# Kernel optimization log

Measured on AMD Instinct MI355X. Metric: run time of the kernel, lower is better.

## Reference

```python
import jax, jax.numpy as jnp
import numpy as np

B, L, E = 4, 2048, 1024
H, DQ, DV = 8, 128, 128
SCALE = 1.0 / np.sqrt(DQ).astype(np.float32)


def setup_inputs() -> dict:
    key = jax.random.key(0)
    ks = jax.random.split(key, 6)
    return {
        "qInputs": jax.random.normal(ks[0], (B, L, E), dtype=jnp.float32),
        "kvInputs": jax.random.normal(ks[1], (B, L, E), dtype=jnp.float32),
        "mask": jnp.zeros((B, H, L, L), dtype=jnp.bool_),
        "W_Q": jax.random.normal(ks[2], (E, H * DQ), dtype=jnp.float32) * 0.02,
        "W_K": jax.random.normal(ks[3], (E, H * DQ), dtype=jnp.float32) * 0.02,
        "W_V": jax.random.normal(ks[4], (E, H * DV), dtype=jnp.float32) * 0.02,
        "W_fc": jax.random.normal(ks[5], (H * DV, E), dtype=jnp.float32) * 0.02,
    }


def reference(qInputs, kvInputs, mask, W_Q, W_K, W_V, W_fc):
    b, lq, _ = qInputs.shape
    lk = kvInputs.shape[1]
    # Projections -> [B, H, L, D]
    Q = (qInputs @ W_Q).reshape(b, lq, H, DQ).transpose(0, 2, 1, 3)
    K = (kvInputs @ W_K).reshape(b, lk, H, DQ).transpose(0, 2, 1, 3)
    V = (kvInputs @ W_V).reshape(b, lk, H, DV).transpose(0, 2, 1, 3)
    # Scaled dot-product with additive mask fill of -1e9
    scores = jnp.einsum("bhqd,bhkd->bhqk", Q, K) * SCALE
    scores = jnp.where(mask, jnp.float32(-1e9), scores)
    attn = jax.nn.softmax(scores, axis=-1)
    ctx = jnp.einsum("bhqk,bhkd->bhqd", attn, V)
    ctx = ctx.transpose(0, 2, 1, 3).reshape(b, lq, H * DV)
    return ctx @ W_fc
```

## Files before the change

### kernel.cpp

```cpp
#include <hip/hip_runtime.h>
#include <stdint.h>

#define LQ 2048
#define EDIM 1024
#define HN 8
#define DH 128
#define BATCH 4
#define SCALE_LOG2E 0.12753785051263942f

typedef short bf16x8 __attribute__((ext_vector_type(8)));
typedef float f32x4 __attribute__((ext_vector_type(4)));
typedef unsigned short u16;
typedef unsigned short u16x4 __attribute__((ext_vector_type(4)));

__device__ __forceinline__ u16 f2bf(float f) {
  union { float f; uint32_t u; } c; c.f = f;
  uint32_t u = c.u;
  return (u16)((u + 0x7fffu + ((u >> 16) & 1u)) >> 16);
}

__device__ __forceinline__ void async16(const void* g, void* l) {
  __builtin_amdgcn_global_load_lds((const __attribute__((address_space(1))) void*)g,
                                   (__attribute__((address_space(3))) void*)l, 16, 0, 0);
}

__device__ __forceinline__ uint32_t lds_b(const u16* p) {
  return (uint32_t)(uintptr_t)(__attribute__((address_space(3))) const u16*)p;
}
__device__ __forceinline__ void ldsr4_issue(bf16x8& d0, bf16x8& d1, bf16x8& d2, bf16x8& d3,
                                            uint32_t a0, uint32_t a1, uint32_t a2, uint32_t a3) {
  asm volatile("ds_read_b128 %0, %4\n\t"
               "ds_read_b128 %1, %5\n\t"
               "ds_read_b128 %2, %6\n\t"
               "ds_read_b128 %3, %7"
               : "=&v"(d0), "=&v"(d1), "=&v"(d2), "=&v"(d3)
               : "v"(a0), "v"(a1), "v"(a2), "v"(a3));
}
template <int N>
__device__ __forceinline__ void lgkm_wait_sb() {
  asm volatile("s_waitcnt lgkmcnt(%0)" :: "n"(N) : "memory");
  __builtin_amdgcn_sched_barrier(0);
}
__device__ __forceinline__ uint32_t cvtpk(float lo, float hi) {
  uint32_t r;
  asm("v_cvt_pk_bf16_f32 %0, %1, %2" : "=v"(r) : "v"(lo), "v"(hi));
  return r;
}
__device__ __forceinline__ void plane_swap(uint32_t& a, uint32_t& b) {
#if __has_builtin(__builtin_amdgcn_permlane32_swap) && __has_builtin(__builtin_amdgcn_permlane16_swap)
  auto r1 = __builtin_amdgcn_permlane32_swap(a, b, false, false);
  auto r2 = __builtin_amdgcn_permlane16_swap(r1[0], r1[1], false, false);
  a = r2[0];
  b = r2[1];
#else
  asm("s_nop 1\n\t"
      "v_permlane32_swap_b32 %0, %1\n\t"
      "s_nop 1\n\t"
      "v_permlane16_swap_b32 %0, %1\n\t"
      "s_nop 1"
      : "+v"(a), "+v"(b));
#endif
}

__global__ __launch_bounds__(256) void prep_kernel(const float* __restrict__ qIn, const float* __restrict__ kvIn,
                                                   const float* __restrict__ w0, const float* __restrict__ w1,
                                                   const float* __restrict__ w2, const float* __restrict__ w3,
                                                   u16* __restrict__ oq, u16* __restrict__ okv,
                                                   u16* __restrict__ o0, u16* __restrict__ o1,
                                                   u16* __restrict__ o2, u16* __restrict__ o3) {
  __shared__ float tile[32][33];
  const int bid = blockIdx.x;
  const int t = threadIdx.x;
  if (bid < 16384) {
    const float* in = (bid >= 8192) ? kvIn : qIn;
    u16* out = (bid >= 8192) ? okv : oq;
    size_t i = (size_t)(bid & 8191) * 256 + t;
    float4 v = ((const float4*)in)[i];
    u16x4 o;
    o.x = f2bf(v.x); o.y = f2bf(v.y); o.z = f2bf(v.z); o.w = f2bf(v.w);
    ((u16x4*)out)[i] = o;
  } else {
    const int idx = bid - 16384;
    const int z = idx >> 10;
    const int rem = idx & 1023;
    const float* in; u16* out;
    switch (z) {
      case 0: in = w0; out = o0; break;
      case 1: in = w1; out = o1; break;
      case 2: in = w2; out = o2; break;
      default: in = w3; out = o3; break;
    }
    const int tx = t & 31, ty = t >> 5;
    const int x0 = (rem & 31) * 32;
    const int y0 = (rem >> 5) * 32;
#pragma unroll
    for (int j = 0; j < 32; j += 8)
      tile[ty + j][tx] = in[(size_t)(y0 + ty + j) * EDIM + x0 + tx];
    __syncthreads();
#pragma unroll
    for (int j = 0; j < 32; j += 8)
      out[(size_t)(x0 + ty + j) * EDIM + (y0 + tx)] = f2bf(tile[tx][ty + j]);
  }
}

struct GemmCore {
  template <typename EpiF>
  static __device__ __forceinline__ void run(const u16* __restrict__ A, const u16* __restrict__ Bt,
                                             int m0, int n0, u16* As, u16* Bs, EpiF epi) {
    const int tid = threadIdx.x;
    const int l = tid & 63;
    const int w = tid >> 6;
    const int wm = (w >> 1) * 64;
    const int wn = (w & 1) * 64;
    const int fm = l & 15;
    const int q4 = l >> 4;
    const int f7 = fm & 7;
    f32x4 acc[4][4] = {};
    for (int k0 = 0; k0 < EDIM; k0 += 64) {
      __syncthreads();
#pragma unroll
      for (int ii = 0; ii < 4; ++ii) {
        const int rloc = w * 32 + ii * 8 + (l >> 3);
        const int cs = (l & 7) ^ (rloc & 7);
        async16(A + (size_t)(m0 + rloc) * EDIM + k0 + cs * 8, &As[(w * 32 + ii * 8) * 64 + l * 8]);
        async16(Bt + (size_t)(n0 + rloc) * EDIM + k0 + cs * 8, &Bs[(w * 32 + ii * 8) * 64 + l * 8]);
      }
      __syncthreads();
#pragma unroll
      for (int ks = 0; ks < 2; ++ks) {
        const int coff = ((ks * 4 + q4) ^ f7) * 8;
        bf16x8 a[4], b[4];
#pragma unroll
        for (int i = 0; i < 4; ++i) a[i] = *(const bf16x8*)&As[(wm + i * 16 + fm) * 64 + coff];
#pragma unroll
        for (int j = 0; j < 4; ++j) b[j] = *(const bf16x8*)&Bs[(wn + j * 16 + fm) * 64 + coff];
#pragma unroll
        for (int i = 0; i < 4; ++i)
#pragma unroll
          for (int j = 0; j < 4; ++j)
            acc[i][j] = __builtin_amdgcn_mfma_f32_16x16x32_bf16(a[i], b[j], acc[i][j], 0, 0, 0);
      }
    }
    const int rr = q4 * 4;
#pragma unroll
    for (int i = 0; i < 4; ++i)
#pragma unroll
      for (int j = 0; j < 4; ++j)
#pragma unroll
        for (int r = 0; r < 4; ++r)
          epi(m0 + wm + i * 16 + rr + r, n0 + wn + j * 16 + fm, acc[i][j][r]);
  }
};

__global__ __launch_bounds__(256) void qkv_gemm(const u16* __restrict__ xq, const u16* __restrict__ xkv,
                                                const u16* __restrict__ WqT, const u16* __restrict__ WkT,
                                                const u16* __restrict__ WvT,
                                                u16* __restrict__ Qb, u16* __restrict__ Kb,
                                                u16* __restrict__ Vt,
                                                const unsigned char* __restrict__ mask,
                                                unsigned char* __restrict__ flags) {
  __shared__ __align__(16) u16 As[128 * 64];
  __shared__ __align__(16) u16 Bs[128 * 64];
  __shared__ int wany[4];
  const int z = blockIdx.z;
  if (z == 3) {
    const int t = threadIdx.x;
    const int unit0 = (blockIdx.x * 8 + blockIdx.y) * 16;
#pragma unroll 1
    for (int u = 0; u < 16; ++u) {
      const int idx = unit0 + u;
      const int bh = idx >> 8;
      const int tile16 = idx & 255;
      const int qt = tile16 >> 4, kt = tile16 & 15;
      const int r = t >> 1;
      const size_t base = ((size_t)bh * LQ + qt * 128 + r) * LQ + kt * 128 + (t & 1) * 64;
      const uint4* p = (const uint4*)(mask + base);
      uint4 a = p[0], c = p[1], d = p[2], e = p[3];
      uint32_t any = a.x | a.y | a.z | a.w | c.x | c.y | c.z | c.w |
                     d.x | d.y | d.z | d.w | e.x | e.y | e.z | e.w;
      int wa = __any(any != 0);
      if ((t & 63) == 0) wany[t >> 6] = wa;
      __syncthreads();
      if (t == 0)
        flags[(size_t)bh * 256 + tile16] = (unsigned char)(wany[0] | wany[1] | wany[2] | wany[3]);
      __syncthreads();
    }
    return;
  }
  if (z == 0) {
    GemmCore::run(xq, WqT, blockIdx.x * 128, blockIdx.y * 128, As, Bs,
                  [&](int gm, int gn, float v) { Qb[(size_t)gm * EDIM + gn] = f2bf(v * SCALE_LOG2E); });
  } else if (z == 1) {
    GemmCore::run(xkv, WkT, blockIdx.x * 128, blockIdx.y * 128, As, Bs,
                  [&](int gm, int gn, float v) { Kb[(size_t)gm * EDIM + gn] = f2bf(v); });
  } else {
    GemmCore::run(WvT, xkv, blockIdx.y * 128, blockIdx.x * 128, As, Bs,
                  [&](int gm, int gn, float v) {
                    Vt[((size_t)(gn >> 11) * 1024 + gm) * 2048 + (gn & 2047)] = f2bf(v);
                  });
  }
}

__global__ __launch_bounds__(256) void out_gemm(const u16* __restrict__ ctx, const u16* __restrict__ WfcT,
                                                float* __restrict__ out) {
  __shared__ __align__(16) u16 As[128 * 64];
  __shared__ __align__(16) u16 Bs[128 * 64];
  GemmCore::run(ctx, WfcT, blockIdx.x * 128, blockIdx.y * 128, As, Bs,
                [&](int gm, int gn, float v) { out[(size_t)gm * EDIM + gn] = v; });
}

__global__ __launch_bounds__(256, 2) void attn_kernel(const u16* __restrict__ Qb, const u16* __restrict__ Kb,
                                                      const u16* __restrict__ Vt,
                                                      const unsigned char* __restrict__ mask,
                                                      const unsigned char* __restrict__ flags,
                                                      u16* __restrict__ ctx) {
  __shared__ __align__(16) u16 Ktile[2][64 * 128];
  __shared__ __align__(16) u16 Vtile[2][128 * 64];
  const int tid = threadIdx.x;
  const int l = tid & 63;
  const int w = tid >> 6;
  const int qt = blockIdx.x;
  const int h = blockIdx.y;
  const int b = blockIdx.z;
  const int fm = l & 15;
  const int q4 = l >> 4;
  const int fk = q4 * 8;
  const int f7 = fm & 7;
  const int qbase = qt * 128 + w * 32;
  const int bh = b * HN + h;

  const u16* Kbh = Kb + (size_t)b * LQ * EDIM + h * DH;
  const u16* Vth = Vt + (size_t)bh * DH * LQ;
  const size_t mbase = (size_t)bh * (size_t)LQ * LQ;

  const unsigned char* tf = flags + (size_t)bh * 256 + qt * 16;
  uint32_t fmask = 0;
#pragma unroll
  for (int i = 0; i < 16; ++i) fmask |= (tf[i] ? 1u : 0u) << i;

  bf16x8 qf[2][4];
#pragma unroll
  for (int mt = 0; mt < 2; ++mt)
#pragma unroll
    for (int ks = 0; ks < 4; ++ks)
      qf[mt][ks] = *(const bf16x8*)(Qb + (size_t)(b * LQ + qbase + mt * 16 + fm) * EDIM + h * DH + ks * 32 + fk);

  auto stageK = [&](int kt_, int buf) {
#pragma unroll
    for (int ii = 0; ii < 4; ++ii) {
      const int i = w * 4 + ii;
      const int row = i * 4 + (l >> 4);
      const int g = (l & 15) ^ (row & 7);
      async16(Kbh + (size_t)(kt_ * 64 + row) * EDIM + g * 8, &Ktile[buf][i * 512 + l * 8]);
    }
  };
  auto stageV = [&](int kt_, int buf) {
#pragma unroll
    for (int ii = 0; ii < 4; ++ii) {
      const int i = w * 4 + ii;
      const int row = i * 8 + (l >> 3);
      const int g = (l & 7) ^ (row & 7);
      async16(Vth + (size_t)row * LQ + kt_ * 64 + g * 8, &Vtile[buf][i * 512 + l * 8]);
    }
  };

  stageK(0, 0);
  stageV(0, 0);

  f32x4 o[2][8] = {};
  float lsumv[2] = {0.f, 0.f};

  for (int it = 0; it < 32; ++it) {
    const int cur = it & 1;
    __syncthreads();
    if (it + 1 < 32) { stageK(it + 1, 1 - cur); stageV(it + 1, 1 - cur); }

    const u16* KT = &Ktile[cur][0];
    const u16* VT = &Vtile[cur][0];

    f32x4 st[4][2] = {};
    bf16x8 kf[2][4];
    {
      const int slot = q4 ^ f7;
      ldsr4_issue(kf[0][0], kf[0][1], kf[0][2], kf[0][3],
                  lds_b(KT + (0 * 16 + fm) * 128 + slot * 8),
                  lds_b(KT + (1 * 16 + fm) * 128 + slot * 8),
                  lds_b(KT + (2 * 16 + fm) * 128 + slot * 8),
                  lds_b(KT + (3 * 16 + fm) * 128 + slot * 8));
    }
#pragma unroll
    for (int ks = 0; ks < 4; ++ks) {
      const int c = ks & 1;
      if (ks + 1 < 4) {
        const int slot = ((ks + 1) * 4 + q4) ^ f7;
        ldsr4_issue(kf[c ^ 1][0], kf[c ^ 1][1], kf[c ^ 1][2], kf[c ^ 1][3],
                    lds_b(KT + (0 * 16 + fm) * 128 + slot * 8),
                    lds_b(KT + (1 * 16 + fm) * 128 + slot * 8),
                    lds_b(KT + (2 * 16 + fm) * 128 + slot * 8),
                    lds_b(KT + (3 * 16 + fm) * 128 + slot * 8));
        lgkm_wait_sb<4>();
      } else {
        lgkm_wait_sb<0>();
      }
      __builtin_amdgcn_s_setprio(1);
#pragma unroll
      for (int mt = 0; mt < 2; ++mt) {
        st[0][mt] = __builtin_amdgcn_mfma_f32_16x16x32_bf16(kf[c][0], qf[mt][ks], st[0][mt], 0, 0, 0);
        st[1][mt] = __builtin_amdgcn_mfma_f32_16x16x32_bf16(kf[c][1], qf[mt][ks], st[1][mt], 0, 0, 0);
        st[2][mt] = __builtin_amdgcn_mfma_f32_16x16x32_bf16(kf[c][2], qf[mt][ks], st[2][mt], 0, 0, 0);
        st[3][mt] = __builtin_amdgcn_mfma_f32_16x16x32_bf16(kf[c][3], qf[mt][ks], st[3][mt], 0, 0, 0);
      }
      __builtin_amdgcn_s_setprio(0);
    }

    const int hasMask = (fmask >> (it >> 1)) & 1;
    uint32_t pk[2][4][2];
#pragma unroll
    for (int mt = 0; mt < 2; ++mt) {
      float sum = 0.f;
      if (hasMask) {
        const unsigned char* mrow = mask + mbase + (size_t)(qbase + mt * 16 + fm) * LQ + it * 64 + q4 * 4;
#pragma unroll
        for (int kt = 0; kt < 4; ++kt) {
          const uint32_t mv = *(const uint32_t*)(mrow + kt * 16);
#pragma unroll
          for (int r = 0; r < 4; ++r) {
            float e = ((mv >> (8 * r)) & 0xffu) ? 0.f : exp2f(st[kt][mt][r]);
            st[kt][mt][r] = e;
            sum += e;
          }
        }
      } else {
#pragma unroll
        for (int kt = 0; kt < 4; ++kt)
#pragma unroll
          for (int r = 0; r < 4; ++r) {
            float e = exp2f(st[kt][mt][r]);
            st[kt][mt][r] = e;
            sum += e;
          }
      }
      sum += __shfl_xor(sum, 16);
      sum += __shfl_xor(sum, 32);
      lsumv[mt] += sum;
#pragma unroll
      for (int kt = 0; kt < 4; ++kt) {
        pk[mt][kt][0] = cvtpk(st[kt][mt][0], st[kt][mt][1]);
        pk[mt][kt][1] = cvtpk(st[kt][mt][2], st[kt][mt][3]);
      }
    }

    {
      bf16x8 v0, v1, v2, v3, v4, v5, v6, v7;
      const int vs0 = q4 ^ f7;
      ldsr4_issue(v0, v1, v2, v3,
                  lds_b(VT + (0 * 16 + fm) * 64 + vs0 * 8), lds_b(VT + (1 * 16 + fm) * 64 + vs0 * 8),
                  lds_b(VT + (2 * 16 + fm) * 64 + vs0 * 8), lds_b(VT + (3 * 16 + fm) * 64 + vs0 * 8));
      ldsr4_issue(v4, v5, v6, v7,
                  lds_b(VT + (4 * 16 + fm) * 64 + vs0 * 8), lds_b(VT + (5 * 16 + fm) * 64 + vs0 * 8),
                  lds_b(VT + (6 * 16 + fm) * 64 + vs0 * 8), lds_b(VT + (7 * 16 + fm) * 64 + vs0 * 8));
      bf16x8 x0, x1, x2, x3, x4, x5, x6, x7;
      const int vs1 = (4 + q4) ^ f7;
      ldsr4_issue(x0, x1, x2, x3,
                  lds_b(VT + (0 * 16 + fm) * 64 + vs1 * 8), lds_b(VT + (1 * 16 + fm) * 64 + vs1 * 8),
                  lds_b(VT + (2 * 16 + fm) * 64 + vs1 * 8), lds_b(VT + (3 * 16 + fm) * 64 + vs1 * 8));
      ldsr4_issue(x4, x5, x6, x7,
                  lds_b(VT + (4 * 16 + fm) * 64 + vs1 * 8), lds_b(VT + (5 * 16 + fm) * 64 + vs1 * 8),
                  lds_b(VT + (6 * 16 + fm) * 64 + vs1 * 8), lds_b(VT + (7 * 16 + fm) * 64 + vs1 * 8));

      bf16x8 paf0, paf1;
      {
        union { uint32_t u[4]; bf16x8 v; } fb;
        uint32_t e0 = pk[0][0][0], f0 = pk[0][1][0];
        uint32_t e1 = pk[0][0][1], f1 = pk[0][1][1];
        plane_swap(e0, f0); plane_swap(e1, f1);
        fb.u[0] = e0; fb.u[1] = e1; fb.u[2] = f0; fb.u[3] = f1;
        paf0 = fb.v;
        uint32_t g0 = pk[1][0][0], h0 = pk[1][1][0];
        uint32_t g1 = pk[1][0][1], h1 = pk[1][1][1];
        plane_swap(g0, h0); plane_swap(g1, h1);
        fb.u[0] = g0; fb.u[1] = g1; fb.u[2] = h0; fb.u[3] = h1;
        paf1 = fb.v;
      }
      lgkm_wait_sb<8>();
      __builtin_amdgcn_s_setprio(1);
      o[0][0] = __builtin_amdgcn_mfma_f32_16x16x32_bf16(paf0, v0, o[0][0], 0, 0, 0);
      o[1][0] = __builtin_amdgcn_mfma_f32_16x16x32_bf16(paf1, v0, o[1][0], 0, 0, 0);
      o[0][1] = __builtin_amdgcn_mfma_f32_16x16x32_bf16(paf0, v1, o[0][1], 0, 0, 0);
      o[1][1] = __builtin_amdgcn_mfma_f32_16x16x32_bf16(paf1, v1, o[1][1], 0, 0, 0);
      o[0][2] = __builtin_amdgcn_mfma_f32_16x16x32_bf16(paf0, v2, o[0][2], 0, 0, 0);
      o[1][2] = __builtin_amdgcn_mfma_f32_16x16x32_bf16(paf1, v2, o[1][2], 0, 0, 0);
      o[0][3] = __builtin_amdgcn_mfma_f32_16x16x32_bf16(paf0, v3, o[0][3], 0, 0, 0);
      o[1][3] = __builtin_amdgcn_mfma_f32_16x16x32_bf16(paf1, v3, o[1][3], 0, 0, 0);
      o[0][4] = __builtin_amdgcn_mfma_f32_16x16x32_bf16(paf0, v4, o[0][4], 0, 0, 0);
      o[1][4] = __builtin_amdgcn_mfma_f32_16x16x32_bf16(paf1, v4, o[1][4], 0, 0, 0);
      o[0][5] = __builtin_amdgcn_mfma_f32_16x16x32_bf16(paf0, v5, o[0][5], 0, 0, 0);
      o[1][5] = __builtin_amdgcn_mfma_f32_16x16x32_bf16(paf1, v5, o[1][5], 0, 0, 0);
      o[0][6] = __builtin_amdgcn_mfma_f32_16x16x32_bf16(paf0, v6, o[0][6], 0, 0, 0);
      o[1][6] = __builtin_amdgcn_mfma_f32_16x16x32_bf16(paf1, v6, o[1][6], 0, 0, 0);
      o[0][7] = __builtin_amdgcn_mfma_f32_16x16x32_bf16(paf0, v7, o[0][7], 0, 0, 0);
      o[1][7] = __builtin_amdgcn_mfma_f32_16x16x32_bf16(paf1, v7, o[1][7], 0, 0, 0);
      __builtin_amdgcn_s_setprio(0);
      {
        union { uint32_t u[4]; bf16x8 v; } fb;
        uint32_t e0 = pk[0][2][0], f0 = pk[0][3][0];
        uint32_t e1 = pk[0][2][1], f1 = pk[0][3][1];
        plane_swap(e0, f0); plane_swap(e1, f1);
        fb.u[0] = e0; fb.u[1] = e1; fb.u[2] = f0; fb.u[3] = f1;
        paf0 = fb.v;
        uint32_t g0 = pk[1][2][0], h0 = pk[1][3][0];
        uint32_t g1 = pk[1][2][1], h1 = pk[1][3][1];
        plane_swap(g0, h0); plane_swap(g1, h1);
        fb.u[0] = g0; fb.u[1] = g1; fb.u[2] = h0; fb.u[3] = h1;
        paf1 = fb.v;
      }
      lgkm_wait_sb<0>();
      __builtin_amdgcn_s_setprio(1);
      o[0][0] = __builtin_amdgcn_mfma_f32_16x16x32_bf16(paf0, x0, o[0][0], 0, 0, 0);
      o[1][0] = __builtin_amdgcn_mfma_f32_16x16x32_bf16(paf1, x0, o[1][0], 0, 0, 0);
      o[0][1] = __builtin_amdgcn_mfma_f32_16x16x32_bf16(paf0, x1, o[0][1], 0, 0, 0);
      o[1][1] = __builtin_amdgcn_mfma_f32_16x16x32_bf16(paf1, x1, o[1][1], 0, 0, 0);
      o[0][2] = __builtin_amdgcn_mfma_f32_16x16x32_bf16(paf0, x2, o[0][2], 0, 0, 0);
      o[1][2] = __builtin_amdgcn_mfma_f32_16x16x32_bf16(paf1, x2, o[1][2], 0, 0, 0);
      o[0][3] = __builtin_amdgcn_mfma_f32_16x16x32_bf16(paf0, x3, o[0][3], 0, 0, 0);
      o[1][3] = __builtin_amdgcn_mfma_f32_16x16x32_bf16(paf1, x3, o[1][3], 0, 0, 0);
      o[0][4] = __builtin_amdgcn_mfma_f32_16x16x32_bf16(paf0, x4, o[0][4], 0, 0, 0);
      o[1][4] = __builtin_amdgcn_mfma_f32_16x16x32_bf16(paf1, x4, o[1][4], 0, 0, 0);
      o[0][5] = __builtin_amdgcn_mfma_f32_16x16x32_bf16(paf0, x5, o[0][5], 0, 0, 0);
      o[1][5] = __builtin_amdgcn_mfma_f32_16x16x32_bf16(paf1, x5, o[1][5], 0, 0, 0);
      o[0][6] = __builtin_amdgcn_mfma_f32_16x16x32_bf16(paf0, x6, o[0][6], 0, 0, 0);
      o[1][6] = __builtin_amdgcn_mfma_f32_16x16x32_bf16(paf1, x6, o[1][6], 0, 0, 0);
      o[0][7] = __builtin_amdgcn_mfma_f32_16x16x32_bf16(paf0, x7, o[0][7], 0, 0, 0);
      o[1][7] = __builtin_amdgcn_mfma_f32_16x16x32_bf16(paf1, x7, o[1][7], 0, 0, 0);
      __builtin_amdgcn_s_setprio(0);
    }
  }

#pragma unroll
  for (int mt = 0; mt < 2; ++mt)
#pragma unroll
    for (int r = 0; r < 4; ++r) {
      float inv = 1.f / __shfl(lsumv[mt], q4 * 4 + r);
      int gq = b * LQ + qbase + mt * 16 + q4 * 4 + r;
#pragma unroll
      for (int dt = 0; dt < 8; ++dt)
        ctx[(size_t)gq * EDIM + h * DH + dt * 16 + fm] = f2bf(o[mt][dt][r] * inv);
    }
}

extern "C" void kernel_launch(void* const* d_in, const int* in_sizes, int n_in,
                              void* d_out, int out_size, void* d_ws, size_t ws_size,
                              hipStream_t stream) {
  const float* qIn = (const float*)d_in[0];
  const float* kvIn = (const float*)d_in[1];
  const unsigned char* mask = (const unsigned char*)d_in[2];
  const float* W_Q = (const float*)d_in[3];
  const float* W_K = (const float*)d_in[4];
  const float* W_V = (const float*)d_in[5];
  const float* W_fc = (const float*)d_in[6];
  float* out = (float*)d_out;

  uint8_t* ws = (uint8_t*)d_ws;
  const size_t MB = 1u << 20;
  u16* xq   = (u16*)(ws);
  u16* xkv  = (u16*)(ws + 16 * MB);
  u16* WqT  = (u16*)(ws + 32 * MB);
  u16* WkT  = (u16*)(ws + 34 * MB);
  u16* WvT  = (u16*)(ws + 36 * MB);
  u16* WfcT = (u16*)(ws + 38 * MB);
  u16* Qb   = (u16*)(ws + 40 * MB);
  u16* Kb   = (u16*)(ws + 56 * MB);
  u16* Vt   = (u16*)(ws + 72 * MB);
  u16* ctx  = (u16*)(ws + 88 * MB);
  unsigned char* flags = (unsigned char*)(ws + 104 * MB);

  prep_kernel<<<20480, 256, 0, stream>>>(qIn, kvIn, W_Q, W_K, W_V, W_fc,
                                         xq, xkv, WqT, WkT, WvT, WfcT);
  qkv_gemm<<<dim3(64, 8, 4), 256, 0, stream>>>(xq, xkv, WqT, WkT, WvT, Qb, Kb, Vt, mask, flags);
  attn_kernel<<<dim3(16, 8, 4), 256, 0, stream>>>(Qb, Kb, Vt, mask, flags, ctx);
  out_gemm<<<dim3(64, 8), 256, 0, stream>>>(ctx, WfcT, out);
}
```

Measured before the change: 829.2 us.

## Split softmax into halves to overlap exp with PV MFMAs; XCD-aware block mapping

Measured after the change: 826.6 us. About the same (-0.3%).

```diff
diff --git a/kernel.cpp b/kernel.cpp
--- a/kernel.cpp
+++ b/kernel.cpp
@@ -59,6 +59,26 @@
       "v_permlane16_swap_b32 %0, %1\n\t"
       "s_nop 1"
       : "+v"(a), "+v"(b));
+#endif
+}
+__device__ __forceinline__ float xorsum16(float x) {
+#if __has_builtin(__builtin_amdgcn_permlane16_swap)
+  union { float f; uint32_t u; } c; c.f = x;
+  auto r = __builtin_amdgcn_permlane16_swap(c.u, c.u, false, false);
+  union { uint32_t u; float f; } a, b; a.u = r[0]; b.u = r[1];
+  return a.f + b.f;
+#else
+  return x + __shfl_xor(x, 16);
+#endif
+}
+__device__ __forceinline__ float xorsum32(float x) {
+#if __has_builtin(__builtin_amdgcn_permlane32_swap)
+  union { float f; uint32_t u; } c; c.f = x;
+  auto r = __builtin_amdgcn_permlane32_swap(c.u, c.u, false, false);
+  union { uint32_t u; float f; } a, b; a.u = r[0]; b.u = r[1];
+  return a.f + b.f;
+#else
+  return x + __shfl_xor(x, 32);
 #endif
 }
 
@@ -219,9 +239,13 @@
   const int tid = threadIdx.x;
   const int l = tid & 63;
   const int w = tid >> 6;
-  const int qt = blockIdx.x;
-  const int h = blockIdx.y;
-  const int b = blockIdx.z;
+  const int flat = blockIdx.x;
+  const int xcd = flat & 7;
+  const int idx = flat >> 3;
+  const int panel = xcd * 4 + (idx >> 4);
+  const int qt = idx & 15;
+  const int h = panel & 7;
+  const int b = panel >> 3;
   const int fm = l & 15;
   const int q4 = l >> 4;
   const int fk = q4 * 8;
@@ -280,6 +304,8 @@
 
     f32x4 st[4][2] = {};
     bf16x8 kf[2][4];
+    bf16x8 v0, v1, v2, v3, v4, v5, v6, v7;
+    bf16x8 x0, x1, x2, x3, x4, x5, x6, x7;
     {
       const int slot = q4 ^ f7;
       ldsr4_issue(kf[0][0], kf[0][1], kf[0][2], kf[0][3],
@@ -289,19 +315,15 @@
                   lds_b(KT + (3 * 16 + fm) * 128 + slot * 8));
     }
 #pragma unroll
-    for (int ks = 0; ks < 4; ++ks) {
+    for (int ks = 0; ks < 3; ++ks) {
       const int c = ks & 1;
-      if (ks + 1 < 4) {
-        const int slot = ((ks + 1) * 4 + q4) ^ f7;
-        ldsr4_issue(kf[c ^ 1][0], kf[c ^ 1][1], kf[c ^ 1][2], kf[c ^ 1][3],
-                    lds_b(KT + (0 * 16 + fm) * 128 + slot * 8),
-                    lds_b(KT + (1 * 16 + fm) * 128 + slot * 8),
-                    lds_b(KT + (2 * 16 + fm) * 128 + slot * 8),
-                    lds_b(KT + (3 * 16 + fm) * 128 + slot * 8));
-        lgkm_wait_sb<4>();
-      } else {
-        lgkm_wait_sb<0>();
-      }
+      const int slot = ((ks + 1) * 4 + q4) ^ f7;
+      ldsr4_issue(kf[c ^ 1][0], kf[c ^ 1][1], kf[c ^ 1][2], kf[c ^ 1][3],
+                  lds_b(KT + (0 * 16 + fm) * 128 + slot * 8),
+                  lds_b(KT + (1 * 16 + fm) * 128 + slot * 8),
+                  lds_b(KT + (2 * 16 + fm) * 128 + slot * 8),
+                  lds_b(KT + (3 * 16 + fm) * 128 + slot * 8));
+      lgkm_wait_sb<4>();
       __builtin_amdgcn_s_setprio(1);
 #pragma unroll
       for (int mt = 0; mt < 2; ++mt) {
@@ -312,16 +334,37 @@
       }
       __builtin_amdgcn_s_setprio(0);
     }
+    {
+      const int vs0 = q4 ^ f7;
+      ldsr4_issue(v0, v1, v2, v3,
+                  lds_b(VT + (0 * 16 + fm) * 64 + vs0 * 8), lds_b(VT + (1 * 16 + fm) * 64 + vs0 * 8),
+                  lds_b(VT + (2 * 16 + fm) * 64 + vs0 * 8), lds_b(VT + (3 * 16 + fm) * 64 + vs0 * 8));
+      ldsr4_issue(v4, v5, v6, v7,
+                  lds_b(VT + (4 * 16 + fm) * 64 + vs0 * 8), lds_b(VT + (5 * 16 + fm) * 64 + vs0 * 8),
+                  lds_b(VT + (6 * 16 + fm) * 64 + vs0 * 8), lds_b(VT + (7 * 16 + fm) * 64 + vs0 * 8));
+      lgkm_wait_sb<8>();
+      __builtin_amdgcn_s_setprio(1);
+#pragma unroll
+      for (int mt = 0; mt < 2; ++mt) {
+        st[0][mt] = __builtin_amdgcn_mfma_f32_16x16x32_bf16(kf[1][0], qf[mt][3], st[0][mt], 0, 0, 0);
+        st[1][mt] = __builtin_amdgcn_mfma_f32_16x16x32_bf16(kf[1][1], qf[mt][3], st[1][mt], 0, 0, 0);
+        st[2][mt] = __builtin_amdgcn_mfma_f32_16x16x32_bf16(kf[1][2], qf[mt][3], st[2][mt], 0, 0, 0);
+        st[3][mt] = __builtin_amdgcn_mfma_f32_16x16x32_bf16(kf[1][3], qf[mt][3], st[3][mt], 0, 0, 0);
+      }
+      __builtin_amdgcn_s_setprio(0);
+    }
 
     const int hasMask = (fmask >> (it >> 1)) & 1;
     uint32_t pk[2][4][2];
+    float sA[2], sB[2];
+    bf16x8 paf0, paf1;
 #pragma unroll
     for (int mt = 0; mt < 2; ++mt) {
       float sum = 0.f;
       if (hasMask) {
         const unsigned char* mrow = mask + mbase + (size_t)(qbase + mt * 16 + fm) * LQ + it * 64 + q4 * 4;
 #pragma unroll
-        for (int kt = 0; kt < 4; ++kt) {
+        for (int kt = 0; kt < 2; ++kt) {
           const uint32_t mv = *(const uint32_t*)(mrow + kt * 16);
 #pragma unroll
           for (int r = 0; r < 4; ++r) {
@@ -332,7 +375,7 @@
         }
       } else {
 #pragma unroll
-        for (int kt = 0; kt < 4; ++kt)
+        for (int kt = 0; kt < 2; ++kt)
 #pragma unroll
           for (int r = 0; r < 4; ++r) {
             float e = exp2f(st[kt][mt][r]);
@@ -340,26 +383,26 @@
             sum += e;
           }
       }
-      sum += __shfl_xor(sum, 16);
-      sum += __shfl_xor(sum, 32);
-      lsumv[mt] += sum;
-#pragma unroll
-      for (int kt = 0; kt < 4; ++kt) {
-        pk[mt][kt][0] = cvtpk(st[kt][mt][0], st[kt][mt][1]);
-        pk[mt][kt][1] = cvtpk(st[kt][mt][2], st[kt][mt][3]);
-      }
-    }
-
+      sA[mt] = sum;
+      pk[mt][0][0] = cvtpk(st[0][mt][0], st[0][mt][1]);
+      pk[mt][0][1] = cvtpk(st[0][mt][2], st[0][mt][3]);
+      pk[mt][1][0] = cvtpk(st[1][mt][0], st[1][mt][1]);
+      pk[mt][1][1] = cvtpk(st[1][mt][2], st[1][mt][3]);
+    }
     {
-      bf16x8 v0, v1, v2, v3, v4, v5, v6, v7;
-      const int vs0 = q4 ^ f7;
-      ldsr4_issue(v0, v1, v2, v3,
-                  lds_b(VT + (0 * 16 + fm) * 64 + vs0 * 8), lds_b(VT + (1 * 16 + fm) * 64 + vs0 * 8),
-                  lds_b(VT + (2 * 16 + fm) * 64 + vs0 * 8), lds_b(VT + (3 * 16 + fm) * 64 + vs0 * 8));
-      ldsr4_issue(v4, v5, v6, v7,
-                  lds_b(VT + (4 * 16 + fm) * 64 + vs0 * 8), lds_b(VT + (5 * 16 + fm) * 64 + vs0 * 8),
-                  lds_b(VT + (6 * 16 + fm) * 64 + vs0 * 8), lds_b(VT + (7 * 16 + fm) * 64 + vs0 * 8));
-      bf16x8 x0, x1, x2, x3, x4, x5, x6, x7;
+      union { uint32_t u[4]; bf16x8 v; } fb;
+      uint32_t e0 = pk[0][0][0], f0 = pk[0][1][0];
+      uint32_t e1 = pk[0][0][1], f1 = pk[0][1][1];
+      plane_swap(e0, f0); plane_swap(e1, f1);
+      fb.u[0] = e0; fb.u[1] = e1; fb.u[2] = f0; fb.u[3] = f1;
+      paf0 = fb.v;
+      uint32_t g0 = pk[1][0][0], h0 = pk[1][1][0];
+      uint32_t g1 = pk[1][0][1], h1 = pk[1][1][1];
+      plane_swap(g0, h0); plane_swap(g1, h1);
+      fb.u[0] = g0; fb.u[1] = g1; fb.u[2] = h0; fb.u[3] = h1;
+      paf1 = fb.v;
+    }
+    {
       const int vs1 = (4 + q4) ^ f7;
       ldsr4_issue(x0, x1, x2, x3,
                   lds_b(VT + (0 * 16 + fm) * 64 + vs1 * 8), lds_b(VT + (1 * 16 + fm) * 64 + vs1 * 8),
@@ -367,73 +410,96 @@
       ldsr4_issue(x4, x5, x6, x7,
                   lds_b(VT + (4 * 16 + fm) * 64 + vs1 * 8), lds_b(VT + (5 * 16 + fm) * 64 + vs1 * 8),
                   lds_b(VT + (6 * 16 + fm) * 64 + vs1 * 8), lds_b(VT + (7 * 16 + fm) * 64 + vs1 * 8));
-
-      bf16x8 paf0, paf1;
-      {
-        union { uint32_t u[4]; bf16x8 v; } fb;
-        uint32_t e0 = pk[0][0][0], f0 = pk[0][1][0];
-        uint32_t e1 = pk[0][0][1], f1 = pk[0][1][1];
-        plane_swap(e0, f0); plane_swap(e1, f1);
-        fb.u[0] = e0; fb.u[1] = e1; fb.u[2] = f0; fb.u[3] = f1;
-        paf0 = fb.v;
-        uint32_t g0 = pk[1][0][0], h0 = pk[1][1][0];
-        uint32_t g1 = pk[1][0][1], h1 = pk[1][1][1];
-        plane_swap(g0, h0); plane_swap(g1, h1);
-        fb.u[0] = g0; fb.u[1] = g1; fb.u[2] = h0; fb.u[3] = h1;
-        paf1 = fb.v;
+    }
+    lgkm_wait_sb<8>();
+    __builtin_amdgcn_s_setprio(1);
+    o[0][0] = __builtin_amdgcn_mfma_f32_16x16x32_bf16(paf0, v0, o[0][0], 0, 0, 0);
+    o[1][0] = __builtin_amdgcn_mfma_f32_16x16x32_bf16(paf1, v0, o[1][0], 0, 0, 0);
+    o[0][1] = __builtin_amdgcn_mfma_f32_16x16x32_bf16(paf0, v1, o[0][1], 0, 0, 0);
+    o[1][1] = __builtin_amdgcn_mfma_f32_16x16x32_bf16(paf1, v1, o[1][1], 0, 0, 0);
+    o[0][2] = __builtin_amdgcn_mfma_f32_16x16x32_bf16(paf0, v2, o[0][2], 0, 0, 0);
+    o[1][2] = __builtin_amdgcn_mfma_f32_16x16x32_bf16(paf1, v2, o[1][2], 0, 0, 0);
+    o[0][3] = __builtin_amdgcn_mfma_f32_16x16x32_bf16(paf0, v3, o[0][3], 0, 0, 0);
+    o[1][3] = __builtin_amdgcn_mfma_f32_16x16x32_bf16(paf1, v3, o[1][3], 0, 0, 0);
+    o[0][4] = __builtin_amdgcn_mfma_f32_16x16x32_bf16(paf0, v4, o[0][4], 0, 0, 0);
+    o[1][4] = __builtin_amdgcn_mfma_f32_16x16x32_bf16(paf1, v4, o[1][4], 0, 0, 0);
+    o[0][5] = __builtin_amdgcn_mfma_f32_16x16x32_bf16(paf0, v5, o[0][5], 0, 0, 0);
+    o[1][5] = __builtin_amdgcn_mfma_f32_16x16x32_bf16(paf1, v5, o[1][5], 0, 0, 0);
+    o[0][6] = __builtin_amdgcn_mfma_f32_16x16x32_bf16(paf0, v6, o[0][6], 0, 0, 0);
+    o[1][6] = __builtin_amdgcn_mfma_f32_16x16x32_bf16(paf1, v6, o[1][6], 0, 0, 0);
+    o[0][7] = __builtin_amdgcn_mfma_f32_16x16x32_bf16(paf0, v7, o[0][7], 0, 0, 0);
+    o[1][7] = __builtin_amdgcn_mfma_f32_16x16x32_bf16(paf1, v7, o[1][7], 0, 0, 0);
+    __builtin_amdgcn_s_setprio(0);
+
+#pragma unroll
+    for (int mt = 0; mt < 2; ++mt) {
+      float sum = 0.f;
+      if (hasMask) {
+        const unsigned char* mrow = mask + mbase + (size_t)(qbase + mt * 16 + fm) * LQ + it * 64 + q4 * 4;
+#pragma unroll
+        for (int kt = 2; kt < 4; ++kt) {
+          const uint32_t mv = *(const uint32_t*)(mrow + kt * 16);
+#pragma unroll
+          for (int r = 0; r < 4; ++r) {
+            float e = ((mv >> (8 * r)) & 0xffu) ? 0.f : exp2f(st[kt][mt][r]);
+            st[kt][mt][r] = e;
+            sum += e;
+          }
+        }
+      } else {
+#pragma unroll
+        for (int kt = 2; kt < 4; ++kt)
+#pragma unroll
+          for (int r = 0; r < 4; ++r) {
+            float e = exp2f(st[kt][mt][r]);
+            st[kt][mt][r] = e;
+            sum += e;
+          }
       }
-      lgkm_wait_sb<8>();
-      __builtin_amdgcn_s_setprio(1);
-      o[0][0] = __builtin_amdgcn_mfma_f32_16x16x32_bf16(paf0, v0, o[0][0], 0, 0, 0);
-      o[1][0] = __builtin_amdgcn_mfma_f32_16x16x32_bf16(paf1, v0, o[1][0], 0, 0, 0);
-      o[0][1] = __builtin_amdgcn_mfma_f32_16x16x32_bf16(paf0, v1, o[0][1], 0, 0, 0);
-      o[1][1] = __builtin_amdgcn_mfma_f32_16x16x32_bf16(paf1, v1, o[1][1], 0, 0, 0);
-      o[0][2] = __builtin_amdgcn_mfma_f32_16x16x32_bf16(paf0, v2, o[0][2], 0, 0, 0);
-      o[1][2] = __builtin_amdgcn_mfma_f32_16x16x32_bf16(paf1, v2, o[1][2], 0, 0, 0);
-      o[0][3] = __builtin_amdgcn_mfma_f32_16x16x32_bf16(paf0, v3, o[0][3], 0, 0, 0);
-      o[1][3] = __builtin_amdgcn_mfma_f32_16x16x32_bf16(paf1, v3, o[1][3], 0, 0, 0);
-      o[0][4] = __builtin_amdgcn_mfma_f32_16x16x32_bf16(paf0, v4, o[0][4], 0, 0, 0);
-      o[1][4] = __builtin_amdgcn_mfma_f32_16x16x32_bf16(paf1, v4, o[1][4], 0, 0, 0);
-      o[0][5] = __builtin_amdgcn_mfma_f32_16x16x32_bf16(paf0, v5, o[0][5], 0, 0, 0);
-      o[1][5] = __builtin_amdgcn_mfma_f32_16x16x32_bf16(paf1, v5, o[1][5], 0, 0, 0);
-      o[0][6] = __builtin_amdgcn_mfma_f32_16x16x32_bf16(paf0, v6, o[0][6], 0, 0, 0);
-      o[1][6] = __builtin_amdgcn_mfma_f32_16x16x32_bf16(paf1, v6, o[1][6], 0, 0, 0);
-      o[0][7] = __builtin_amdgcn_mfma_f32_16x16x32_bf16(paf0, v7, o[0][7], 0, 0, 0);
-      o[1][7] = __builtin_amdgcn_mfma_f32_16x16x32_bf16(paf1, v7, o[1][7], 0, 0, 0);
-      __builtin_amdgcn_s_setprio(0);
-      {
-        union { uint32_t u[4]; bf16x8 v; } fb;
-        uint32_t e0 = pk[0][2][0], f0 = pk[0][3][0];
-        uint32_t e1 = pk[0][2][1], f1 = pk[0][3][1];
-        plane_swap(e0, f0); plane_swap(e1, f1);
-        fb.u[0] = e0; fb.u[1] = e1; fb.u[2] = f0; fb.u[3] = f1;
-        paf0 = fb.v;
-        uint32_t g0 = pk[1][2][0], h0 = pk[1][3][0];
-        uint32_t g1 = pk[1][2][1], h1 = pk[1][3][1];
-        plane_swap(g0, h0); plane_swap(g1, h1);
-        fb.u[0] = g0; fb.u[1] = g1; fb.u[2] = h0; fb.u[3] = h1;
-        paf1 = fb.v;
-      }
-      lgkm_wait_sb<0>();
-      __builtin_amdgcn_s_setprio(1);
-      o[0][0] = __builtin_amdgcn_mfma_f32_16x16x32_bf16(paf0, x0, o[0][0], 0, 0, 0);
-      o[1][0] = __builtin_amdgcn_mfma_f32_16x16x32_bf16(paf1, x0, o[1][0], 0, 0, 0);
-      o[0][1] = __builtin_amdgcn_mfma_f32_16x16x32_bf16(paf0, x1, o[0][1], 0, 0, 0);
-      o[1][1] = __builtin_amdgcn_mfma_f32_16x16x32_bf16(paf1, x1, o[1][1], 0, 0, 0);
-      o[0][2] = __builtin_amdgcn_mfma_f32_16x16x32_bf16(paf0, x2, o[0][2], 0, 0, 0);
-      o[1][2] = __builtin_amdgcn_mfma_f32_16x16x32_bf16(paf1, x2, o[1][2], 0, 0, 0);
-      o[0][3] = __builtin_amdgcn_mfma_f32_16x16x32_bf16(paf0, x3, o[0][3], 0, 0, 0);
-      o[1][3] = __builtin_amdgcn_mfma_f32_16x16x32_bf16(paf1, x3, o[1][3], 0, 0, 0);
-      o[0][4] = __builtin_amdgcn_mfma_f32_16x16x32_bf16(paf0, x4, o[0][4], 0, 0, 0);
-      o[1][4] = __builtin_amdgcn_mfma_f32_16x16x32_bf16(paf1, x4, o[1][4], 0, 0, 0);
-      o[0][5] = __builtin_amdgcn_mfma_f32_16x16x32_bf16(paf0, x5, o[0][5], 0, 0, 0);
-      o[1][5] = __builtin_amdgcn_mfma_f32_16x16x32_bf16(paf1, x5, o[1][5], 0, 0, 0);
-      o[0][6] = __builtin_amdgcn_mfma_f32_16x16x32_bf16(paf0, x6, o[0][6], 0, 0, 0);
-      o[1][6] = __builtin_amdgcn_mfma_f32_16x16x32_bf16(paf1, x6, o[1][6], 0, 0, 0);
-      o[0][7] = __builtin_amdgcn_mfma_f32_16x16x32_bf16(paf0, x7, o[0][7], 0, 0, 0);
-      o[1][7] = __builtin_amdgcn_mfma_f32_16x16x32_bf16(paf1, x7, o[1][7], 0, 0, 0);
-      __builtin_amdgcn_s_setprio(0);
-    }
+      sB[mt] = sum;
+      pk[mt][2][0] = cvtpk(st[2][mt][0], st[2][mt][1]);
+      pk[mt][2][1] = cvtpk(st[2][mt][2], st[2][mt][3]);
+      pk[mt][3][0] = cvtpk(st[3][mt][0], st[3][mt][1]);
+      pk[mt][3][1] = cvtpk(st[3][mt][2], st[3][mt][3]);
+    }
+    {
+      union { uint32_t u[4]; bf16x8 v; } fb;
+      uint32_t e0 = pk[0][2][0], f0 = pk[0][3][0];
+      uint32_t e1 = pk[0][2][1], f1 = pk[0][3][1];
+      plane_swap(e0, f0); plane_swap(e1, f1);
+      fb.u[0] = e0; fb.u[1] = e1; fb.u[2] = f0; fb.u[3] = f1;
+      paf0 = fb.v;
+      uint32_t g0 = pk[1][2][0], h0 = pk[1][3][0];
+      uint32_t g1 = pk[1][2][1], h1 = pk[1][3][1];
+      plane_swap(g0, h0); plane_swap(g1, h1);
+      fb.u[0] = g0; fb.u[1] = g1; fb.u[2] = h0; fb.u[3] = h1;
+      paf1 = fb.v;
+    }
+#pragma unroll
+    for (int mt = 0; mt < 2; ++mt) {
+      float t = sA[mt] + sB[mt];
+      lsumv[mt] += xorsum32(xorsum16(t));
+    }
+
+    lgkm_wait_sb<0>();
+    __builtin_amdgcn_s_setprio(1);
+    o[0][0] = __builtin_amdgcn_mfma_f32_16x16x32_bf16(paf0, x0, o[0][0], 0, 0, 0);
+    o[1][0] = __builtin_amdgcn_mfma_f32_16x16x32_bf16(paf1, x0, o[1][0], 0, 0, 0);
+    o[0][1] = __builtin_amdgcn_mfma_f32_16x16x32_bf16(paf0, x1, o[0][1], 0, 0, 0);
+    o[1][1] = __builtin_amdgcn_mfma_f32_16x16x32_bf16(paf1, x1, o[1][1], 0, 0, 0);
+    o[0][2] = __builtin_amdgcn_mfma_f32_16x16x32_bf16(paf0, x2, o[0][2], 0, 0, 0);
+    o[1][2] = __builtin_amdgcn_mfma_f32_16x16x32_bf16(paf1, x2, o[1][2], 0, 0, 0);
+    o[0][3] = __builtin_amdgcn_mfma_f32_16x16x32_bf16(paf0, x3, o[0][3], 0, 0, 0);
+    o[1][3] = __builtin_amdgcn_mfma_f32_16x16x32_bf16(paf1, x3, o[1][3], 0, 0, 0);
+    o[0][4] = __builtin_amdgcn_mfma_f32_16x16x32_bf16(paf0, x4, o[0][4], 0, 0, 0);
+    o[1][4] = __builtin_amdgcn_mfma_f32_16x16x32_bf16(paf1, x4, o[1][4], 0, 0, 0);
+    o[0][5] = __builtin_amdgcn_mfma_f32_16x16x32_bf16(paf0, x5, o[0][5], 0, 0, 0);
+    o[1][5] = __builtin_amdgcn_mfma_f32_16x16x32_bf16(paf1, x5, o[1][5], 0, 0, 0);
+    o[0][6] = __builtin_amdgcn_mfma_f32_16x16x32_bf16(paf0, x6, o[0][6], 0, 0, 0);
+    o[1][6] = __builtin_amdgcn_mfma_f32_16x16x32_bf16(paf1, x6, o[1][6], 0, 0, 0);
+    o[0][7] = __builtin_amdgcn_mfma_f32_16x16x32_bf16(paf0, x7, o[0][7], 0, 0, 0);
+    o[1][7] = __builtin_amdgcn_mfma_f32_16x16x32_bf16(paf1, x7, o[1][7], 0, 0, 0);
+    __builtin_amdgcn_s_setprio(0);
   }
 
 #pragma unroll
@@ -477,6 +543,6 @@
   prep_kernel<<<20480, 256, 0, stream>>>(qIn, kvIn, W_Q, W_K, W_V, W_fc,
                                          xq, xkv, WqT, WkT, WvT, WfcT);
   qkv_gemm<<<dim3(64, 8, 4), 256, 0, stream>>>(xq, xkv, WqT, WkT, WvT, Qb, Kb, Vt, mask, flags);
-  attn_kernel<<<dim3(16, 8, 4), 256, 0, stream>>>(Qb, Kb, Vt, mask, flags, ctx);
+  attn_kernel<<<512, 256, 0, stream>>>(Qb, Kb, Vt, mask, flags, ctx);
   out_gemm<<<dim3(64, 8), 256, 0, stream>>>(ctx, WfcT, out);
 }
```
